# Performance work log

Hardware: AMD Instinct MI355X
Metric: run time of the kernel (lower is better)

Reference implementation:

```python
import jax, jax.numpy as jnp
import numpy as np

B, T, N_EMBD, HEAD = 4, 4096, 1024, 64


def setup_inputs() -> dict:
    key = jax.random.key(0)
    k1, k2, k3, k4 = jax.random.split(key, 4)
    x = jax.random.normal(k1, (B, T, N_EMBD), dtype=jnp.float32)
    # nn.Linear weights, stored as [in, out] so y = x @ W
    s = 1.0 / np.sqrt(N_EMBD)
    Wq = jax.random.uniform(k2, (N_EMBD, HEAD), dtype=jnp.float32, minval=-s, maxval=s)
    Wk = jax.random.uniform(k3, (N_EMBD, HEAD), dtype=jnp.float32, minval=-s, maxval=s)
    Wv = jax.random.uniform(k4, (N_EMBD, HEAD), dtype=jnp.float32, minval=-s, maxval=s)
    return {"x": x, "Wq": Wq, "Wk": Wk, "Wv": Wv}


def reference(x, Wq, Wk, Wv):
    # x: [B, T, C] with C = n_embd; note: original scales by sqrt(C), not sqrt(head_size)
    T_, C = x.shape[1], x.shape[2]
    q = x @ Wq            # [B, T, H]
    k = x @ Wk            # [B, T, H]
    v = x @ Wv            # [B, T, H]
    scale = 1.0 / jnp.sqrt(jnp.asarray(C, dtype=x.dtype))
    w = jnp.einsum('bqh,bkh->bqk', q, k) * scale  # [B, T, T]
    causal = jnp.tril(jnp.ones((T_, T_), dtype=bool))
    w = jnp.where(causal, w, -jnp.inf)
    attn = jax.nn.softmax(w, axis=-1)
    # dropout in eval mode (identity) for deterministic reference
    return attn @ v       # [B, T, H]
```

## Files before the change

kernel.cpp:

```cpp
#include <hip/hip_runtime.h>

constexpr int B_  = 4;
constexpr int T_  = 4096;
constexpr int C_  = 1024;
constexpr int H_  = 64;
constexpr int BT_ = B_ * T_;
constexpr int NUNIT_ = 1152;

typedef __attribute__((ext_vector_type(4))) float f32x4;
typedef __attribute__((ext_vector_type(8))) short bf16x8;
typedef __attribute__((ext_vector_type(8))) unsigned short u16x8;
typedef __attribute__((ext_vector_type(4))) unsigned short u16x4;
typedef __attribute__((ext_vector_type(2))) unsigned int u32x2;

__device__ __forceinline__ unsigned short f32_to_bf16(float f) {
    union { float f; unsigned int u; } v;
    v.f = f;
    unsigned int r = v.u + 0x7FFFu + ((v.u >> 16) & 1u);
    return (unsigned short)(r >> 16);
}
__device__ __forceinline__ float bf16_to_f32(unsigned short us) {
    union { unsigned int u; float f; } v;
    v.u = (unsigned int)us << 16;
    return v.f;
}
__device__ __forceinline__ float exp2_hw(float x) {
    return __builtin_amdgcn_exp2f(x);
}
__device__ __forceinline__ unsigned int cvt_pk_bf16(float lo, float hi) {
    unsigned int r;
    asm("v_cvt_pk_bf16_f32 %0, %1, %2" : "=v"(r) : "v"(lo), "v"(hi));
    return r;
}

__global__ __launch_bounds__(256) void wconv_kernel(
    const float* __restrict__ Wq, const float* __restrict__ Wk,
    const float* __restrict__ Wv, unsigned short* __restrict__ Wt)
{
    const int tid  = threadIdx.x;
    const int wid  = blockIdx.x * 4 + (tid >> 6);
    const int lane = tid & 63;
    const int q    = lane >> 4, c = lane & 15;
    const int ntile = wid >> 5;
    const int kstep = wid & 31;
    const int n = ntile * 16 + c;
    const int m = n >> 6;
    const float* W = (m == 0) ? Wq : (m == 1) ? Wk : Wv;
    const int ncol = n & 63;
    const int k0 = kstep * 32 + q * 8;
    u16x8 pk;
#pragma unroll
    for (int j = 0; j < 8; j++) pk[j] = f32_to_bf16(W[(size_t)(k0 + j) * H_ + ncol]);
    *(u16x8*)(Wt + (size_t)wid * 512 + lane * 8) = pk;
}

__global__ __launch_bounds__(256, 4) void proj_kernel(
    const float* __restrict__ x, const unsigned short* __restrict__ Wt,
    unsigned short* __restrict__ Qf, unsigned short* __restrict__ Kf,
    unsigned short* __restrict__ Vf)
{
    __shared__ __align__(16) unsigned short xs[16][16][72];
    const int t    = threadIdx.x;
    const int r0   = blockIdx.x * 16;
    const int w    = t >> 6;
    const int lane = t & 63;
    const int quad = lane >> 4;
    const int c    = lane & 15;
    const int nh   = w * 48;
    const int row  = t >> 4;
    const int koff = (t & 15) * 4;

    const float* xp = x + (size_t)(r0 + row) * C_ + koff;
    f32x4 xv[16];
#pragma unroll
    for (int p = 0; p < 16; p++) xv[p] = *(const f32x4*)(xp + 64 * p);
#pragma unroll
    for (int p = 0; p < 16; p++) {
        u16x4 pk;
#pragma unroll
        for (int i = 0; i < 4; i++) pk[i] = f32_to_bf16(xv[p][i]);
        *(u16x4*)&xs[p][row][koff] = pk;
    }
    __syncthreads();

    f32x4 acc[3];
#pragma unroll
    for (int j = 0; j < 3; j++) acc[j] = {0.f, 0.f, 0.f, 0.f};

#pragma unroll
    for (int p = 0; p < 16; p++) {
#pragma unroll
        for (int ks = 0; ks < 64; ks += 32) {
            const bf16x8 a0 = *(const bf16x8*)&xs[p][c][ks + quad * 8];
            const unsigned short* bp =
                Wt + ((size_t)(nh >> 4) * 32 + ((p * 64 + ks) >> 5)) * 512 + lane * 8;
#pragma unroll
            for (int j = 0; j < 3; j++) {
                const bf16x8 bj = *(const bf16x8*)(bp + (size_t)j * 32 * 512);
                acc[j] = __builtin_amdgcn_mfma_f32_16x16x32_bf16(a0, bj, acc[j], 0, 0, 0);
            }
        }
    }

    const int S   = r0;
    const int bS  = S >> 12;
    const int cc0 = quad * 4;
#pragma unroll
    for (int j = 0; j < 3; j++) {
        const int nt = nh + j * 16;
        if (nt < 128) {
            const int d0 = (nt < 64) ? nt : nt - 64;
            unsigned short* base = (nt < 64) ? Qf : Kf;
            const int t16  = (S & 4095) >> 4;
            const int half = d0 >> 5;
            const int q8   = ((d0 >> 4) & 1) * 2 + (c >> 3);
            const int j8   = c & 7;
            unsigned short* pq = base + ((size_t)(bS * 256 + t16)) * 1024
                               + half * 512 + q8 * 128 + j8;
#pragma unroll
            for (int r = 0; r < 4; r++) pq[(cc0 + r) * 8] = f32_to_bf16(acc[j][r]);
        } else {
            const int d0  = nt - 128;
            const int k32 = (S & 4095) >> 5;
            const int ht  = d0 >> 4;
            const int sq  = (S & 31) >> 3;
            unsigned short* pv = Vf + (((size_t)(bS * 128 + k32)) * 4 + ht) * 512 + c * 8;
#pragma unroll
            for (int r = 0; r < 4; r++) {
                const int cc = cc0 + r;
                pv[(sq + (cc >> 3)) * 128 + (cc & 7)] = f32_to_bf16(acc[j][r]);
            }
        }
    }
}

__global__ __launch_bounds__(256) void attn_kernel(
    const unsigned short* __restrict__ Qf, const unsigned short* __restrict__ Kf,
    const unsigned short* __restrict__ Vf, unsigned short* __restrict__ Opg,
    float* __restrict__ mlg)
{
    __shared__ __align__(16) unsigned short Pb[4][16][72];
    const int tid  = threadIdx.x;
    const int w    = tid >> 6;
    const int lane = tid & 63;
    const int quad = lane >> 4;
    const int c    = lane & 15;
    const int bid  = blockIdx.x;
    const int qt   = 255 - (bid & 255);
    const int ks   = bid >> 8;
    const int g    = qt >> 5;
    if (ks > g) return;
    const int b    = w;
    const int q0   = qt * 16;
    const int k0   = ks * 512;
    const int kend = (q0 + 15 < k0 + 511) ? q0 + 15 : k0 + 511;

    const unsigned short* qp = Qf + ((size_t)b * 256 + qt) * 1024 + lane * 8;
    const bf16x8 qB0 = *(const bf16x8*)qp;
    const bf16x8 qB1 = *(const bf16x8*)(qp + 512);

    f32x4 O[4];
#pragma unroll
    for (int tt = 0; tt < 4; tt++) O[tt] = {0.f, 0.f, 0.f, 0.f};
    float m = -1e30f, ls = 0.f;
    const float scale2 = 0.045084436f;

    unsigned short* P = &Pb[w][0][0];
    const int prow = c * 72;

    bf16x8 kC[8];
    {
        const unsigned short* kfb = Kf + ((size_t)b * 256 + (k0 >> 4)) * 1024 + lane * 8;
#pragma unroll
        for (int i = 0; i < 4; i++) {
            kC[2 * i]     = *(const bf16x8*)(kfb + i * 1024);
            kC[2 * i + 1] = *(const bf16x8*)(kfb + i * 1024 + 512);
        }
    }

    for (int kb = k0; kb <= kend; kb += 64) {
        f32x4 S[4];
        __builtin_amdgcn_s_setprio(1);
#pragma unroll
        for (int tt = 0; tt < 4; tt++) {
            f32x4 s = {0.f, 0.f, 0.f, 0.f};
            s = __builtin_amdgcn_mfma_f32_16x16x32_bf16(kC[2 * tt],     qB0, s, 0, 0, 0);
            s = __builtin_amdgcn_mfma_f32_16x16x32_bf16(kC[2 * tt + 1], qB1, s, 0, 0, 0);
            S[tt] = s;
        }
        __builtin_amdgcn_s_setprio(0);
        if (kb + 64 <= kend) {
            const unsigned short* kfb =
                Kf + ((size_t)b * 256 + ((kb + 64) >> 4)) * 1024 + lane * 8;
#pragma unroll
            for (int i = 0; i < 4; i++) {
                kC[2 * i]     = *(const bf16x8*)(kfb + i * 1024);
                kC[2 * i + 1] = *(const bf16x8*)(kfb + i * 1024 + 512);
            }
        }
        const unsigned short* vfb = Vf + ((size_t)b * 128 + (kb >> 5)) * 2048 + lane * 8;
        const bf16x8 vC0 = *(const bf16x8*)(vfb + 0 * 512);
        const bf16x8 vC1 = *(const bf16x8*)(vfb + 1 * 512);
        const bf16x8 vC2 = *(const bf16x8*)(vfb + 2 * 512);
        const bf16x8 vC3 = *(const bf16x8*)(vfb + 3 * 512);
        const bf16x8 vC4 = *(const bf16x8*)(vfb + 2048 + 0 * 512);
        const bf16x8 vC5 = *(const bf16x8*)(vfb + 2048 + 1 * 512);
        const bf16x8 vC6 = *(const bf16x8*)(vfb + 2048 + 2 * 512);
        const bf16x8 vC7 = *(const bf16x8*)(vfb + 2048 + 3 * 512);

        if (kb + 63 > q0) {
#pragma unroll
            for (int tt = 0; tt < 4; tt++)
#pragma unroll
                for (int r = 0; r < 4; r++) {
                    const int key = kb + tt * 16 + quad * 4 + r;
                    if (key > q0 + c) S[tt][r] = -1e30f;
                }
        }

        float t0 = fmaxf(fmaxf(S[0][0], S[0][1]), fmaxf(S[0][2], S[0][3]));
        float t1 = fmaxf(fmaxf(S[1][0], S[1][1]), fmaxf(S[1][2], S[1][3]));
        float t2 = fmaxf(fmaxf(S[2][0], S[2][1]), fmaxf(S[2][2], S[2][3]));
        float t3 = fmaxf(fmaxf(S[3][0], S[3][1]), fmaxf(S[3][2], S[3][3]));
        float mx = fmaxf(fmaxf(t0, t1), fmaxf(t2, t3));
        mx = fmaxf(mx, __shfl_xor(mx, 16));
        mx = fmaxf(mx, __shfl_xor(mx, 32));
        const float mxs = mx * scale2;

        if (__any(mxs > m)) {
            const float mn    = fmaxf(m, mxs);
            const float alpha = exp2_hw(m - mn);
            m = mn;
            ls *= alpha;
#pragma unroll
            for (int tt = 0; tt < 4; tt++)
#pragma unroll
                for (int r = 0; r < 4; r++) O[tt][r] *= alpha;
        }

        float lp0 = 0.f, lp1 = 0.f, lp2 = 0.f, lp3 = 0.f;
#pragma unroll
        for (int tt = 0; tt < 4; tt++) {
            const float e0 = exp2_hw(fmaf(S[tt][0], scale2, -m));
            const float e1 = exp2_hw(fmaf(S[tt][1], scale2, -m));
            const float e2 = exp2_hw(fmaf(S[tt][2], scale2, -m));
            const float e3 = exp2_hw(fmaf(S[tt][3], scale2, -m));
            const float l  = (e0 + e1) + (e2 + e3);
            if (tt == 0) lp0 = l; else if (tt == 1) lp1 = l;
            else if (tt == 2) lp2 = l; else lp3 = l;
            u32x2 pw;
            pw[0] = cvt_pk_bf16(e0, e1);
            pw[1] = cvt_pk_bf16(e2, e3);
            *(u32x2*)(P + prow + tt * 16 + quad * 4) = pw;
        }
        ls += (lp0 + lp1) + (lp2 + lp3);

        const bf16x8 pB0 = *(const bf16x8*)(P + prow + quad * 8);
        const bf16x8 pB1 = *(const bf16x8*)(P + prow + 32 + quad * 8);

        __builtin_amdgcn_s_setprio(1);
        O[0] = __builtin_amdgcn_mfma_f32_16x16x32_bf16(vC0, pB0, O[0], 0, 0, 0);
        O[0] = __builtin_amdgcn_mfma_f32_16x16x32_bf16(vC4, pB1, O[0], 0, 0, 0);
        O[1] = __builtin_amdgcn_mfma_f32_16x16x32_bf16(vC1, pB0, O[1], 0, 0, 0);
        O[1] = __builtin_amdgcn_mfma_f32_16x16x32_bf16(vC5, pB1, O[1], 0, 0, 0);
        O[2] = __builtin_amdgcn_mfma_f32_16x16x32_bf16(vC2, pB0, O[2], 0, 0, 0);
        O[2] = __builtin_amdgcn_mfma_f32_16x16x32_bf16(vC6, pB1, O[2], 0, 0, 0);
        O[3] = __builtin_amdgcn_mfma_f32_16x16x32_bf16(vC3, pB0, O[3], 0, 0, 0);
        O[3] = __builtin_amdgcn_mfma_f32_16x16x32_bf16(vC7, pB1, O[3], 0, 0, 0);
        __builtin_amdgcn_s_setprio(0);
    }

    ls += __shfl_xor(ls, 16);
    ls += __shfl_xor(ls, 32);

    const size_t ustore = (size_t)b * NUNIT_ + qt + 16 * g * (g - 1) + g * (qt & 31) + ks;
#pragma unroll
    for (int tt = 0; tt < 4; tt++) {
        u32x2 pw;
        pw[0] = cvt_pk_bf16(O[tt][0], O[tt][1]);
        pw[1] = cvt_pk_bf16(O[tt][2], O[tt][3]);
        *(u32x2*)(Opg + ustore * 1024 + c * 64 + tt * 16 + quad * 4) = pw;
    }
    if (lane < 16) {
        mlg[ustore * 32 + c]      = m;
        mlg[ustore * 32 + 16 + c] = ls;
    }
}

__global__ __launch_bounds__(256) void merge_kernel(
    const unsigned short* __restrict__ Opg, const float* __restrict__ mlg,
    float* __restrict__ out)
{
    const int idx = blockIdx.x;
    const int b   = idx >> 8;
    const int qt  = idx & 255;
    const int g   = qt >> 5;
    const int nseg = g + 1;
    const size_t base = (size_t)b * NUNIT_ + qt + 16 * g * (g - 1) + g * (qt & 31);
    const int t  = threadIdx.x;
    const int h  = t & 63;
    const int rg = t >> 6;
#pragma unroll
    for (int i = 0; i < 4; i++) {
        const int row = rg * 4 + i;
        float M = -1e30f;
        for (int s = 0; s < nseg; s++) M = fmaxf(M, mlg[(base + s) * 32 + row]);
        float L = 0.f, val = 0.f;
        for (int s = 0; s < nseg; s++) {
            const float e = exp2_hw(mlg[(base + s) * 32 + row] - M);
            L   = fmaf(mlg[(base + s) * 32 + 16 + row], e, L);
            val = fmaf(bf16_to_f32(Opg[(base + s) * 1024 + row * 64 + h]), e, val);
        }
        out[((size_t)b * T_ + qt * 16 + row) * H_ + h] = val / L;
    }
}

extern "C" void kernel_launch(void* const* d_in, const int* in_sizes, int n_in,
                              void* d_out, int out_size, void* d_ws, size_t ws_size,
                              hipStream_t stream) {
    const float* x  = (const float*)d_in[0];
    const float* Wq = (const float*)d_in[1];
    const float* Wk = (const float*)d_in[2];
    const float* Wv = (const float*)d_in[3];
    float* out = (float*)d_out;

    unsigned short* Qf = (unsigned short*)d_ws;
    unsigned short* Kf = Qf + (size_t)BT_ * H_;
    unsigned short* Vf = Kf + (size_t)BT_ * H_;
    unsigned short* Wt = Vf + (size_t)BT_ * H_;
    unsigned short* Opg = Wt + (size_t)192 * C_;
    float*          mlg = (float*)(Opg + (size_t)B_ * NUNIT_ * 1024);

    wconv_kernel<<<96, 256, 0, stream>>>(Wq, Wk, Wv, Wt);
    proj_kernel<<<1024, 256, 0, stream>>>(x, Wt, Qf, Kf, Vf);
    attn_kernel<<<2048, 256, 0, stream>>>(Qf, Kf, Vf, Opg, mlg);
    merge_kernel<<<1024, 256, 0, stream>>>(Opg, mlg, out);
}
```

Before: 157.1 us.

## Fuse projection and attention into one kernel with atomic segment-ready counters

Projection and attention are merged into a single persistent-style kernel. The first 256 blocks each project 64 rows, ordered by a chain of atomic counters, and every block then processes attention work units, spinning until the K/V segments it needs have been published. The intent is to remove a kernel launch boundary and let attention on early segments overlap with projection of later ones. The cost is spin-wait polling, reliance on blocks being co-resident so the waits cannot deadlock, and relaxed-ordering visibility concerns. Projection is also now spread over fewer, serialized blocks.

```diff
diff --git a/kernel.cpp b/kernel.cpp
--- a/kernel.cpp
+++ b/kernel.cpp
@@ -35,9 +35,11 @@
 
 __global__ __launch_bounds__(256) void wconv_kernel(
     const float* __restrict__ Wq, const float* __restrict__ Wk,
-    const float* __restrict__ Wv, unsigned short* __restrict__ Wt)
+    const float* __restrict__ Wv, unsigned short* __restrict__ Wt,
+    unsigned int* __restrict__ segcnt)
 {
     const int tid  = threadIdx.x;
+    if (blockIdx.x == 0 && tid < 32) segcnt[tid] = 0;
     const int wid  = blockIdx.x * 4 + (tid >> 6);
     const int lane = tid & 63;
     const int q    = lane >> 4, c = lane & 15;
@@ -54,236 +56,258 @@
     *(u16x8*)(Wt + (size_t)wid * 512 + lane * 8) = pk;
 }
 
-__global__ __launch_bounds__(256, 4) void proj_kernel(
+__global__ __launch_bounds__(256, 4) void fused_kernel(
     const float* __restrict__ x, const unsigned short* __restrict__ Wt,
     unsigned short* __restrict__ Qf, unsigned short* __restrict__ Kf,
-    unsigned short* __restrict__ Vf)
+    unsigned short* __restrict__ Vf, unsigned short* __restrict__ Opg,
+    float* __restrict__ mlg, unsigned int* __restrict__ segcnt)
 {
     __shared__ __align__(16) unsigned short xs[16][16][72];
+    const int bid  = blockIdx.x;
     const int t    = threadIdx.x;
-    const int r0   = blockIdx.x * 16;
     const int w    = t >> 6;
     const int lane = t & 63;
     const int quad = lane >> 4;
     const int c    = lane & 15;
-    const int nh   = w * 48;
-    const int row  = t >> 4;
-    const int koff = (t & 15) * 4;
-
-    const float* xp = x + (size_t)(r0 + row) * C_ + koff;
-    f32x4 xv[16];
-#pragma unroll
-    for (int p = 0; p < 16; p++) xv[p] = *(const f32x4*)(xp + 64 * p);
-#pragma unroll
-    for (int p = 0; p < 16; p++) {
-        u16x4 pk;
-#pragma unroll
-        for (int i = 0; i < 4; i++) pk[i] = f32_to_bf16(xv[p][i]);
-        *(u16x4*)&xs[p][row][koff] = pk;
+
+    if (bid < 256) {
+        const int pb = bid >> 6;
+        if (pb > 0) {
+            for (;;) {
+                unsigned int done = 0;
+#pragma unroll
+                for (int s = 0; s < 8; ++s)
+                    done += __hip_atomic_load(&segcnt[(pb - 1) * 8 + s],
+                                              __ATOMIC_RELAXED, __HIP_MEMORY_SCOPE_AGENT);
+                if (done >= 64) break;
+                __builtin_amdgcn_s_sleep(32);
+            }
+            __builtin_amdgcn_sched_barrier(0);
+        }
+        const int nh   = w * 48;
+        const int row  = t >> 4;
+        const int koff = (t & 15) * 4;
+
+        for (int pp = 0; pp < 4; ++pp) {
+            const int r0 = (bid * 4 + pp) * 16;
+            const float* xp = x + (size_t)(r0 + row) * C_ + koff;
+            f32x4 xv[16];
+#pragma unroll
+            for (int p = 0; p < 16; p++) xv[p] = *(const f32x4*)(xp + 64 * p);
+            if (pp) __syncthreads();
+#pragma unroll
+            for (int p = 0; p < 16; p++) {
+                u16x4 pk;
+#pragma unroll
+                for (int i = 0; i < 4; i++) pk[i] = f32_to_bf16(xv[p][i]);
+                *(u16x4*)&xs[p][row][koff] = pk;
+            }
+            __syncthreads();
+
+            f32x4 acc[3];
+#pragma unroll
+            for (int j = 0; j < 3; j++) acc[j] = {0.f, 0.f, 0.f, 0.f};
+#pragma unroll
+            for (int p = 0; p < 16; p++) {
+#pragma unroll
+                for (int ks = 0; ks < 64; ks += 32) {
+                    const bf16x8 a0 = *(const bf16x8*)&xs[p][c][ks + quad * 8];
+                    const unsigned short* bp =
+                        Wt + ((size_t)(nh >> 4) * 32 + ((p * 64 + ks) >> 5)) * 512 + lane * 8;
+#pragma unroll
+                    for (int j = 0; j < 3; j++) {
+                        const bf16x8 bj = *(const bf16x8*)(bp + (size_t)j * 32 * 512);
+                        acc[j] = __builtin_amdgcn_mfma_f32_16x16x32_bf16(a0, bj, acc[j], 0, 0, 0);
+                    }
+                }
+            }
+            const int S   = r0;
+            const int bS  = S >> 12;
+            const int cc0 = quad * 4;
+#pragma unroll
+            for (int j = 0; j < 3; j++) {
+                const int nt = nh + j * 16;
+                if (nt < 128) {
+                    const int d0 = (nt < 64) ? nt : nt - 64;
+                    unsigned short* base = (nt < 64) ? Qf : Kf;
+                    const int t16  = (S & 4095) >> 4;
+                    const int half = d0 >> 5;
+                    const int q8   = ((d0 >> 4) & 1) * 2 + (c >> 3);
+                    const int j8   = c & 7;
+                    unsigned short* pq = base + ((size_t)(bS * 256 + t16)) * 1024
+                                       + half * 512 + q8 * 128 + j8;
+#pragma unroll
+                    for (int r = 0; r < 4; r++) pq[(cc0 + r) * 8] = f32_to_bf16(acc[j][r]);
+                } else {
+                    const int d0  = nt - 128;
+                    const int k32 = (S & 4095) >> 5;
+                    const int ht  = d0 >> 4;
+                    const int sq  = (S & 31) >> 3;
+                    unsigned short* pv = Vf + (((size_t)(bS * 128 + k32)) * 4 + ht) * 512 + c * 8;
+#pragma unroll
+                    for (int r = 0; r < 4; r++) {
+                        const int cc = cc0 + r;
+                        pv[(sq + (cc >> 3)) * 128 + (cc & 7)] = f32_to_bf16(acc[j][r]);
+                    }
+                }
+            }
+        }
+        __syncthreads();
+        if (t == 0) {
+            __threadfence();
+            atomicAdd(&segcnt[bid >> 3], 1u);
+        }
     }
-    __syncthreads();
-
-    f32x4 acc[3];
-#pragma unroll
-    for (int j = 0; j < 3; j++) acc[j] = {0.f, 0.f, 0.f, 0.f};
-
-#pragma unroll
-    for (int p = 0; p < 16; p++) {
-#pragma unroll
-        for (int ks = 0; ks < 64; ks += 32) {
-            const bf16x8 a0 = *(const bf16x8*)&xs[p][c][ks + quad * 8];
-            const unsigned short* bp =
-                Wt + ((size_t)(nh >> 4) * 32 + ((p * 64 + ks) >> 5)) * 512 + lane * 8;
-#pragma unroll
-            for (int j = 0; j < 3; j++) {
-                const bf16x8 bj = *(const bf16x8*)(bp + (size_t)j * 32 * 512);
-                acc[j] = __builtin_amdgcn_mfma_f32_16x16x32_bf16(a0, bj, acc[j], 0, 0, 0);
-            }
-        }
-    }
-
-    const int S   = r0;
-    const int bS  = S >> 12;
-    const int cc0 = quad * 4;
-#pragma unroll
-    for (int j = 0; j < 3; j++) {
-        const int nt = nh + j * 16;
-        if (nt < 128) {
-            const int d0 = (nt < 64) ? nt : nt - 64;
-            unsigned short* base = (nt < 64) ? Qf : Kf;
-            const int t16  = (S & 4095) >> 4;
-            const int half = d0 >> 5;
-            const int q8   = ((d0 >> 4) & 1) * 2 + (c >> 3);
-            const int j8   = c & 7;
-            unsigned short* pq = base + ((size_t)(bS * 256 + t16)) * 1024
-                               + half * 512 + q8 * 128 + j8;
-#pragma unroll
-            for (int r = 0; r < 4; r++) pq[(cc0 + r) * 8] = f32_to_bf16(acc[j][r]);
-        } else {
-            const int d0  = nt - 128;
-            const int k32 = (S & 4095) >> 5;
-            const int ht  = d0 >> 4;
-            const int sq  = (S & 31) >> 3;
-            unsigned short* pv = Vf + (((size_t)(bS * 128 + k32)) * 4 + ht) * 512 + c * 8;
-#pragma unroll
-            for (int r = 0; r < 4; r++) {
-                const int cc = cc0 + r;
-                pv[(sq + (cc >> 3)) * 128 + (cc & 7)] = f32_to_bf16(acc[j][r]);
-            }
-        }
-    }
-}
-
-__global__ __launch_bounds__(256) void attn_kernel(
-    const unsigned short* __restrict__ Qf, const unsigned short* __restrict__ Kf,
-    const unsigned short* __restrict__ Vf, unsigned short* __restrict__ Opg,
-    float* __restrict__ mlg)
-{
-    __shared__ __align__(16) unsigned short Pb[4][16][72];
-    const int tid  = threadIdx.x;
-    const int w    = tid >> 6;
-    const int lane = tid & 63;
-    const int quad = lane >> 4;
-    const int c    = lane & 15;
-    const int bid  = blockIdx.x;
-    const int qt   = 255 - (bid & 255);
-    const int ks   = bid >> 8;
-    const int g    = qt >> 5;
-    if (ks > g) return;
-    const int b    = w;
-    const int q0   = qt * 16;
-    const int k0   = ks * 512;
-    const int kend = (q0 + 15 < k0 + 511) ? q0 + 15 : k0 + 511;
-
-    const unsigned short* qp = Qf + ((size_t)b * 256 + qt) * 1024 + lane * 8;
-    const bf16x8 qB0 = *(const bf16x8*)qp;
-    const bf16x8 qB1 = *(const bf16x8*)(qp + 512);
-
-    f32x4 O[4];
-#pragma unroll
-    for (int tt = 0; tt < 4; tt++) O[tt] = {0.f, 0.f, 0.f, 0.f};
-    float m = -1e30f, ls = 0.f;
+
+    const int slot = (bid >= 256) ? ((bid - 256) * 4 + w) : (3072 + bid * 4 + w);
     const float scale2 = 0.045084436f;
-
-    unsigned short* P = &Pb[w][0][0];
+    unsigned short* P = &xs[0][0][0] + w * 1152;
     const int prow = c * 72;
 
-    bf16x8 kC[8];
-    {
-        const unsigned short* kfb = Kf + ((size_t)b * 256 + (k0 >> 4)) * 1024 + lane * 8;
-#pragma unroll
-        for (int i = 0; i < 4; i++) {
-            kC[2 * i]     = *(const bf16x8*)(kfb + i * 1024);
-            kC[2 * i + 1] = *(const bf16x8*)(kfb + i * 1024 + 512);
-        }
-    }
-
-    for (int kb = k0; kb <= kend; kb += 64) {
-        f32x4 S[4];
-        __builtin_amdgcn_s_setprio(1);
-#pragma unroll
-        for (int tt = 0; tt < 4; tt++) {
-            f32x4 s = {0.f, 0.f, 0.f, 0.f};
-            s = __builtin_amdgcn_mfma_f32_16x16x32_bf16(kC[2 * tt],     qB0, s, 0, 0, 0);
-            s = __builtin_amdgcn_mfma_f32_16x16x32_bf16(kC[2 * tt + 1], qB1, s, 0, 0, 0);
-            S[tt] = s;
-        }
-        __builtin_amdgcn_s_setprio(0);
-        if (kb + 64 <= kend) {
-            const unsigned short* kfb =
-                Kf + ((size_t)b * 256 + ((kb + 64) >> 4)) * 1024 + lane * 8;
+    for (int pass = 0; pass < 2; ++pass) {
+        const int j  = slot + pass * 4096;
+        const int b  = j >> 11;
+        const int ks = (j >> 8) & 7;
+        const int qt = 255 - (j & 255);
+        const int g  = qt >> 5;
+        if (ks > g) continue;
+
+        const int f1 = b * 8 + ks, f2 = b * 8 + g;
+        while (__hip_atomic_load(&segcnt[f1], __ATOMIC_RELAXED, __HIP_MEMORY_SCOPE_AGENT) < 8u ||
+               __hip_atomic_load(&segcnt[f2], __ATOMIC_RELAXED, __HIP_MEMORY_SCOPE_AGENT) < 8u)
+            __builtin_amdgcn_s_sleep(32);
+        __builtin_amdgcn_sched_barrier(0);
+
+        const int q0   = qt * 16;
+        const int k0   = ks * 512;
+        const int kend = (q0 + 15 < k0 + 511) ? q0 + 15 : k0 + 511;
+
+        const unsigned short* qp = Qf + ((size_t)b * 256 + qt) * 1024 + lane * 8;
+        const bf16x8 qB0 = *(const bf16x8*)qp;
+        const bf16x8 qB1 = *(const bf16x8*)(qp + 512);
+
+        f32x4 O[4];
+#pragma unroll
+        for (int tt = 0; tt < 4; tt++) O[tt] = {0.f, 0.f, 0.f, 0.f};
+        float m = -1e30f, ls = 0.f;
+
+        bf16x8 kC[8];
+        {
+            const unsigned short* kfb = Kf + ((size_t)b * 256 + (k0 >> 4)) * 1024 + lane * 8;
 #pragma unroll
             for (int i = 0; i < 4; i++) {
                 kC[2 * i]     = *(const bf16x8*)(kfb + i * 1024);
                 kC[2 * i + 1] = *(const bf16x8*)(kfb + i * 1024 + 512);
             }
         }
-        const unsigned short* vfb = Vf + ((size_t)b * 128 + (kb >> 5)) * 2048 + lane * 8;
-        const bf16x8 vC0 = *(const bf16x8*)(vfb + 0 * 512);
-        const bf16x8 vC1 = *(const bf16x8*)(vfb + 1 * 512);
-        const bf16x8 vC2 = *(const bf16x8*)(vfb + 2 * 512);
-        const bf16x8 vC3 = *(const bf16x8*)(vfb + 3 * 512);
-        const bf16x8 vC4 = *(const bf16x8*)(vfb + 2048 + 0 * 512);
-        const bf16x8 vC5 = *(const bf16x8*)(vfb + 2048 + 1 * 512);
-        const bf16x8 vC6 = *(const bf16x8*)(vfb + 2048 + 2 * 512);
-        const bf16x8 vC7 = *(const bf16x8*)(vfb + 2048 + 3 * 512);
-
-        if (kb + 63 > q0) {
-#pragma unroll
-            for (int tt = 0; tt < 4; tt++)
-#pragma unroll
-                for (int r = 0; r < 4; r++) {
-                    const int key = kb + tt * 16 + quad * 4 + r;
-                    if (key > q0 + c) S[tt][r] = -1e30f;
+
+        for (int kb = k0; kb <= kend; kb += 64) {
+            f32x4 S[4];
+            __builtin_amdgcn_s_setprio(1);
+#pragma unroll
+            for (int tt = 0; tt < 4; tt++) {
+                f32x4 s = {0.f, 0.f, 0.f, 0.f};
+                s = __builtin_amdgcn_mfma_f32_16x16x32_bf16(kC[2 * tt],     qB0, s, 0, 0, 0);
+                s = __builtin_amdgcn_mfma_f32_16x16x32_bf16(kC[2 * tt + 1], qB1, s, 0, 0, 0);
+                S[tt] = s;
+            }
+            __builtin_amdgcn_s_setprio(0);
+            if (kb + 64 <= kend) {
+                const unsigned short* kfb =
+                    Kf + ((size_t)b * 256 + ((kb + 64) >> 4)) * 1024 + lane * 8;
+#pragma unroll
+                for (int i = 0; i < 4; i++) {
+                    kC[2 * i]     = *(const bf16x8*)(kfb + i * 1024);
+                    kC[2 * i + 1] = *(const bf16x8*)(kfb + i * 1024 + 512);
                 }
-        }
-
-        float t0 = fmaxf(fmaxf(S[0][0], S[0][1]), fmaxf(S[0][2], S[0][3]));
-        float t1 = fmaxf(fmaxf(S[1][0], S[1][1]), fmaxf(S[1][2], S[1][3]));
-        float t2 = fmaxf(fmaxf(S[2][0], S[2][1]), fmaxf(S[2][2], S[2][3]));
-        float t3 = fmaxf(fmaxf(S[3][0], S[3][1]), fmaxf(S[3][2], S[3][3]));
-        float mx = fmaxf(fmaxf(t0, t1), fmaxf(t2, t3));
-        mx = fmaxf(mx, __shfl_xor(mx, 16));
-        mx = fmaxf(mx, __shfl_xor(mx, 32));
-        const float mxs = mx * scale2;
-
-        if (__any(mxs > m)) {
-            const float mn    = fmaxf(m, mxs);
-            const float alpha = exp2_hw(m - mn);
-            m = mn;
-            ls *= alpha;
-#pragma unroll
-            for (int tt = 0; tt < 4; tt++)
-#pragma unroll
-                for (int r = 0; r < 4; r++) O[tt][r] *= alpha;
-        }
-
-        float lp0 = 0.f, lp1 = 0.f, lp2 = 0.f, lp3 = 0.f;
+            }
+            const unsigned short* vfb = Vf + ((size_t)b * 128 + (kb >> 5)) * 2048 + lane * 8;
+            const bf16x8 vC0 = *(const bf16x8*)(vfb + 0 * 512);
+            const bf16x8 vC1 = *(const bf16x8*)(vfb + 1 * 512);
+            const bf16x8 vC2 = *(const bf16x8*)(vfb + 2 * 512);
+            const bf16x8 vC3 = *(const bf16x8*)(vfb + 3 * 512);
+            const bf16x8 vC4 = *(const bf16x8*)(vfb + 2048 + 0 * 512);
+            const bf16x8 vC5 = *(const bf16x8*)(vfb + 2048 + 1 * 512);
+            const bf16x8 vC6 = *(const bf16x8*)(vfb + 2048 + 2 * 512);
+            const bf16x8 vC7 = *(const bf16x8*)(vfb + 2048 + 3 * 512);
+
+            if (kb + 63 > q0) {
+#pragma unroll
+                for (int tt = 0; tt < 4; tt++)
+#pragma unroll
+                    for (int r = 0; r < 4; r++) {
+                        const int key = kb + tt * 16 + quad * 4 + r;
+                        if (key > q0 + c) S[tt][r] = -1e30f;
+                    }
+            }
+
+            float t0 = fmaxf(fmaxf(S[0][0], S[0][1]), fmaxf(S[0][2], S[0][3]));
+            float t1 = fmaxf(fmaxf(S[1][0], S[1][1]), fmaxf(S[1][2], S[1][3]));
+            float t2 = fmaxf(fmaxf(S[2][0], S[2][1]), fmaxf(S[2][2], S[2][3]));
+            float t3 = fmaxf(fmaxf(S[3][0], S[3][1]), fmaxf(S[3][2], S[3][3]));
+            float mx = fmaxf(fmaxf(t0, t1), fmaxf(t2, t3));
+            mx = fmaxf(mx, __shfl_xor(mx, 16));
+            mx = fmaxf(mx, __shfl_xor(mx, 32));
+            const float mxs = mx * scale2;
+
+            if (__any(mxs > m)) {
+                const float mn    = fmaxf(m, mxs);
+                const float alpha = exp2_hw(m - mn);
+                m = mn;
+                ls *= alpha;
+#pragma unroll
+                for (int tt = 0; tt < 4; tt++)
+#pragma unroll
+                    for (int r = 0; r < 4; r++) O[tt][r] *= alpha;
+            }
+
+            float lp0 = 0.f, lp1 = 0.f, lp2 = 0.f, lp3 = 0.f;
+#pragma unroll
+            for (int tt = 0; tt < 4; tt++) {
+                const float e0 = exp2_hw(fmaf(S[tt][0], scale2, -m));
+                const float e1 = exp2_hw(fmaf(S[tt][1], scale2, -m));
+                const float e2 = exp2_hw(fmaf(S[tt][2], scale2, -m));
+                const float e3 = exp2_hw(fmaf(S[tt][3], scale2, -m));
+                const float l  = (e0 + e1) + (e2 + e3);
+                if (tt == 0) lp0 = l; else if (tt == 1) lp1 = l;
+                else if (tt == 2) lp2 = l; else lp3 = l;
+                u32x2 pw;
+                pw[0] = cvt_pk_bf16(e0, e1);
+                pw[1] = cvt_pk_bf16(e2, e3);
+                *(u32x2*)(P + prow + tt * 16 + quad * 4) = pw;
+            }
+            ls += (lp0 + lp1) + (lp2 + lp3);
+
+            const bf16x8 pB0 = *(const bf16x8*)(P + prow + quad * 8);
+            const bf16x8 pB1 = *(const bf16x8*)(P + prow + 32 + quad * 8);
+
+            __builtin_amdgcn_s_setprio(1);
+            O[0] = __builtin_amdgcn_mfma_f32_16x16x32_bf16(vC0, pB0, O[0], 0, 0, 0);
+            O[0] = __builtin_amdgcn_mfma_f32_16x16x32_bf16(vC4, pB1, O[0], 0, 0, 0);
+            O[1] = __builtin_amdgcn_mfma_f32_16x16x32_bf16(vC1, pB0, O[1], 0, 0, 0);
+            O[1] = __builtin_amdgcn_mfma_f32_16x16x32_bf16(vC5, pB1, O[1], 0, 0, 0);
+            O[2] = __builtin_amdgcn_mfma_f32_16x16x32_bf16(vC2, pB0, O[2], 0, 0, 0);
+            O[2] = __builtin_amdgcn_mfma_f32_16x16x32_bf16(vC6, pB1, O[2], 0, 0, 0);
+            O[3] = __builtin_amdgcn_mfma_f32_16x16x32_bf16(vC3, pB0, O[3], 0, 0, 0);
+            O[3] = __builtin_amdgcn_mfma_f32_16x16x32_bf16(vC7, pB1, O[3], 0, 0, 0);
+            __builtin_amdgcn_s_setprio(0);
+        }
+
+        ls += __shfl_xor(ls, 16);
+        ls += __shfl_xor(ls, 32);
+
+        const size_t ustore = (size_t)b * NUNIT_ + qt + 16 * g * (g - 1) + g * (qt & 31) + ks;
 #pragma unroll
         for (int tt = 0; tt < 4; tt++) {
-            const float e0 = exp2_hw(fmaf(S[tt][0], scale2, -m));
-            const float e1 = exp2_hw(fmaf(S[tt][1], scale2, -m));
-            const float e2 = exp2_hw(fmaf(S[tt][2], scale2, -m));
-            const float e3 = exp2_hw(fmaf(S[tt][3], scale2, -m));
-            const float l  = (e0 + e1) + (e2 + e3);
-            if (tt == 0) lp0 = l; else if (tt == 1) lp1 = l;
-            else if (tt == 2) lp2 = l; else lp3 = l;
             u32x2 pw;
-            pw[0] = cvt_pk_bf16(e0, e1);
-            pw[1] = cvt_pk_bf16(e2, e3);
-            *(u32x2*)(P + prow + tt * 16 + quad * 4) = pw;
-        }
-        ls += (lp0 + lp1) + (lp2 + lp3);
-
-        const bf16x8 pB0 = *(const bf16x8*)(P + prow + quad * 8);
-        const bf16x8 pB1 = *(const bf16x8*)(P + prow + 32 + quad * 8);
-
-        __builtin_amdgcn_s_setprio(1);
-        O[0] = __builtin_amdgcn_mfma_f32_16x16x32_bf16(vC0, pB0, O[0], 0, 0, 0);
-        O[0] = __builtin_amdgcn_mfma_f32_16x16x32_bf16(vC4, pB1, O[0], 0, 0, 0);
-        O[1] = __builtin_amdgcn_mfma_f32_16x16x32_bf16(vC1, pB0, O[1], 0, 0, 0);
-        O[1] = __builtin_amdgcn_mfma_f32_16x16x32_bf16(vC5, pB1, O[1], 0, 0, 0);
-        O[2] = __builtin_amdgcn_mfma_f32_16x16x32_bf16(vC2, pB0, O[2], 0, 0, 0);
-        O[2] = __builtin_amdgcn_mfma_f32_16x16x32_bf16(vC6, pB1, O[2], 0, 0, 0);
-        O[3] = __builtin_amdgcn_mfma_f32_16x16x32_bf16(vC3, pB0, O[3], 0, 0, 0);
-        O[3] = __builtin_amdgcn_mfma_f32_16x16x32_bf16(vC7, pB1, O[3], 0, 0, 0);
-        __builtin_amdgcn_s_setprio(0);
-    }
-
-    ls += __shfl_xor(ls, 16);
-    ls += __shfl_xor(ls, 32);
-
-    const size_t ustore = (size_t)b * NUNIT_ + qt + 16 * g * (g - 1) + g * (qt & 31) + ks;
-#pragma unroll
-    for (int tt = 0; tt < 4; tt++) {
-        u32x2 pw;
-        pw[0] = cvt_pk_bf16(O[tt][0], O[tt][1]);
-        pw[1] = cvt_pk_bf16(O[tt][2], O[tt][3]);
-        *(u32x2*)(Opg + ustore * 1024 + c * 64 + tt * 16 + quad * 4) = pw;
-    }
-    if (lane < 16) {
-        mlg[ustore * 32 + c]      = m;
-        mlg[ustore * 32 + 16 + c] = ls;
+            pw[0] = cvt_pk_bf16(O[tt][0], O[tt][1]);
+            pw[1] = cvt_pk_bf16(O[tt][2], O[tt][3]);
+            *(u32x2*)(Opg + ustore * 1024 + c * 64 + tt * 16 + quad * 4) = pw;
+        }
+        if (lane < 16) {
+            mlg[ustore * 32 + c]      = m;
+            mlg[ustore * 32 + 16 + c] = ls;
+        }
     }
 }
 
@@ -330,9 +354,9 @@
     unsigned short* Wt = Vf + (size_t)BT_ * H_;
     unsigned short* Opg = Wt + (size_t)192 * C_;
     float*          mlg = (float*)(Opg + (size_t)B_ * NUNIT_ * 1024);
-
-    wconv_kernel<<<96, 256, 0, stream>>>(Wq, Wk, Wv, Wt);
-    proj_kernel<<<1024, 256, 0, stream>>>(x, Wt, Qf, Kf, Vf);
-    attn_kernel<<<2048, 256, 0, stream>>>(Qf, Kf, Vf, Opg, mlg);
+    unsigned int*   segcnt = (unsigned int*)(mlg + (size_t)B_ * NUNIT_ * 32);
+
+    wconv_kernel<<<96, 256, 0, stream>>>(Wq, Wk, Wv, Wt, segcnt);
+    fused_kernel<<<1024, 256, 0, stream>>>(x, Wt, Qf, Kf, Vf, Opg, mlg, segcnt);
     merge_kernel<<<1024, 256, 0, stream>>>(Opg, mlg, out);
 }
```

Result: slower. 601.7 us (+283.1%).
